# Kernel tuning notes

Hardware: AMD Instinct MI355X
Metric: run time of the kernel (lower is better)

## Reference

```python
import jax, jax.numpy as jnp
import numpy as np
from jax import lax

PI = jnp.pi
KX = jnp.array([[-1, 0, 1], [-2, 0, 2], [-1, 0, 1]], jnp.float32)
KY = jnp.array([[-1, -2, -1], [0, 0, 0], [1, 2, 1]], jnp.float32)
K45 = jnp.array([[-2, -1, 0], [-1, 0, 1], [0, 1, 2]], jnp.float32)
K135 = jnp.array([[0, 1, 2], [-1, 0, 1], [-2, -1, 0]], jnp.float32)


def _shift(x, dx, dy):
    # result[i, j] = x[clip(i - dx), clip(j - dy)]  (replicate boundary),
    # exactly matching the torch slice + replicate-pad neighbor construction.
    H, W = x.shape[2], x.shape[3]
    ri = jnp.clip(jnp.arange(H) - dx, 0, H - 1)
    ci = jnp.clip(jnp.arange(W) - dy, 0, W - 1)
    return x[:, :, ri[:, None], ci[None, :]]


def _adaptive_smoothing(f, k=10.0, iter_num=3):
    neighbors = [(-1, -1), (-1, 0), (-1, 1), (0, -1), (0, 0), (0, 1), (1, -1), (1, 0), (1, 1)]
    for _ in range(iter_num):
        Gx = (_shift(f, -1, 0) - _shift(f, 1, 0)) * 0.5   # gradient along H
        Gy = (_shift(f, 0, -1) - _shift(f, 0, 1)) * 0.5   # gradient along W
        w = jnp.exp(-(Gx * Gx + Gy * Gy) / (2.0 * k * k))
        f_new = jnp.zeros_like(f)
        w_sum = jnp.zeros_like(f)
        for dx, dy in neighbors:
            f_new = f_new + _shift(f, dx, dy) * _shift(w, dx, dy)
            w_sum = w_sum + _shift(w, dx, dy)
        f = f_new / jnp.maximum(w_sum, 1e-8)
    return f


def _dwconv(x, k2d):
    # depthwise 3x3 cross-correlation, zero padding (torch Conv2d semantics)
    C = x.shape[1]
    kern = jnp.broadcast_to(k2d[None, None], (C, 1, 3, 3)).astype(x.dtype)
    return lax.conv_general_dilated(x, kern, (1, 1), ((1, 1), (1, 1)),
                                    dimension_numbers=('NCHW', 'OIHW', 'NCHW'),
                                    feature_group_count=C)


def _sobel(x):
    return 0.5 * jnp.abs(_dwconv(x, KX)) + 0.5 * jnp.abs(_dwconv(x, KY))


def _hardswish(x):
    return x * jnp.clip(x + 3.0, 0.0, 6.0) / 6.0


def _canny(data, sigma, weight):
    blurred = _adaptive_smoothing(data, k=10.0, iter_num=3)
    sob = _sobel(blurred)
    B, C, H, W = sob.shape
    # torch.median: lower median = sorted[(n-1)//2]; .item() detaches it
    flat = jnp.sort(sob.reshape(B, C, H * W), axis=-1)
    med = lax.stop_gradient(jnp.mean(flat[:, :, (H * W - 1) // 2]))
    low = jnp.clip((1.0 - sigma) * med, 0.001, 1.0)
    high = jnp.clip((1.0 + sigma) * med, 0.001, 1.0)

    ex = _dwconv(blurred, KX)
    ey = _dwconv(blurred, KY)
    e45 = _dwconv(blurred, K45)
    e135 = _dwconv(blurred, K135)
    mag = jnp.sqrt(ex * ex + ey * ey + e45 * e45 + e135 * e135)
    ang = jnp.mod(jnp.arctan2(ey, ex), PI)

    dirs = jnp.array([0.0, PI / 4, PI / 2, 3 * PI / 4], jnp.float32)
    d = jnp.abs(ang[..., None] - dirs)
    dir_w = jax.nn.softmax(-jnp.minimum(d, PI - d) / 0.01, axis=-1)  # (B,C,H,W,4)

    pm = jnp.pad(mag, ((0, 0), (0, 0), (1, 1), (1, 1)), mode='edge')
    neigh = [(pm[:, :, 1:-1, :-2], pm[:, :, 1:-1, 2:]),
             (pm[:, :, :-2, :-2], pm[:, :, 2:, 2:]),
             (pm[:, :, :-2, 1:-1], pm[:, :, 2:, 1:-1]),
             (pm[:, :, :-2, 2:], pm[:, :, 2:, :-2])]
    sup = jnp.zeros_like(mag)
    for i, (n1, n2) in enumerate(neigh):  # fixed 4-direction loop
        sw = jax.nn.softmax(jnp.stack([mag, n1, n2], axis=-1) / 0.1, axis=-1)[..., 0]
        sup = sup + mag * sw * dir_w[..., i]

    mx = jnp.max(sup)
    sup = sup / jnp.where(mx > 0, mx, 1.0)

    Sh = _hardswish(sup - high)
    Sl = _hardswish(sup - low)
    ecanny = sup * (Sh + Sl)
    dilated = _dwconv(Sh, jnp.ones((3, 3), jnp.float32))
    result = ecanny + dilated * Sl * (1.0 - Sh)

    # enhance_edges with the ORIGINAL input
    result = (1.0 - weight) * result + weight * _sobel(data)
    rmin = jnp.min(result)
    rmax = jnp.max(result)
    return (result - rmin) / (rmax - rmin)


def setup_inputs() -> dict:
    key = jax.random.key(0)
    k1, k2 = jax.random.split(key)
    B, C, H, W = 8, 1, 512, 512
    return {
        'img1': jax.random.uniform(k1, (B, C, H, W), dtype=jnp.float32),
        'img2': jax.random.uniform(k2, (B, C, H, W), dtype=jnp.float32),
        'sigma1': jnp.float32(2.2),
        'enhance_weight1': jnp.float32(0.0),
        'sigma2': jnp.float32(2.2),
        'enhance_weight2': jnp.float32(0.0),
    }


def reference(img1, img2, sigma1, enhance_weight1, sigma2, enhance_weight2):
    s1 = 1.0 - jax.nn.sigmoid(sigma1)
    w1 = jax.nn.sigmoid(enhance_weight1)
    s2 = 1.0 - jax.nn.sigmoid(sigma2)
    w2 = jax.nn.sigmoid(enhance_weight2)
    m1 = _canny(img1, s1, w1)
    m2 = _canny(img2, s2, w2)
    f = (1.0 - m1) * (1.0 - m2) + m1 * m2
    return (1.0 - f, m1, m2)
```

## Files before the change

kernel.cpp:

```cpp
#include <hip/hip_runtime.h>

namespace {

constexpr int H = 512;
constexpr int W = 512;
constexpr int HW = H * W;
constexpr int PPS = 8;
constexpr int NP = 16;
constexpr int TX = 64;
constexpr int TY = 16;
constexpr int STY = 16;
constexpr int NBLK = (W / TX) * (H / TY) * NP;
constexpr float PI_F = 3.14159265358979323846f;
constexpr int NBINS = 1024;
constexpr float BIN_SCALE = 512.0f;

__device__ __forceinline__ float hsw(float x) {
    float t = fminf(fmaxf(x + 3.0f, 0.0f), 6.0f);
    return x * t * (1.0f / 6.0f);
}

__device__ __forceinline__ const float* plane_ptr(const float* s1, const float* s2, int p) {
    return (p < PPS) ? (s1 + (size_t)p * HW) : (s2 + (size_t)(p - PPS) * HW);
}

__device__ __forceinline__ float wave_max(float v) {
    for (int o = 32; o > 0; o >>= 1) v = fmaxf(v, __shfl_down(v, o, 64));
    return v;
}
__device__ __forceinline__ float wave_min(float v) {
    for (int o = 32; o > 0; o >>= 1) v = fminf(v, __shfl_down(v, o, 64));
    return v;
}

__device__ __forceinline__ float atan_poly(float t) {
    float z = t * t;
    float p = -0.01172120f;
    p = p * z + 0.05265332f;
    p = p * z - 0.11643287f;
    p = p * z + 0.19354346f;
    p = p * z - 0.33262347f;
    p = p * z + 0.99997726f;
    return t * p;
}

__device__ __forceinline__ float sel4(int idx, float v0, float v1, float v2, float v3) {
    float a = (idx & 1) ? v1 : v0;
    float b = (idx & 1) ? v3 : v2;
    return (idx & 2) ? b : a;
}

__global__ void K_smooth(const float* __restrict__ s1, const float* __restrict__ s2,
                         float* __restrict__ fout, unsigned* __restrict__ hist) {
    int tid = threadIdx.y * 64 + threadIdx.x;
    if (hist) {
        int bid = (blockIdx.z * gridDim.y + blockIdx.y) * gridDim.x + blockIdx.x;
        if (bid < (NP * NBINS) / 256) hist[bid * 256 + tid] = 0;
    }
    int p = blockIdx.z;
    const float* f = plane_ptr(s1, s2, p);
    int j0 = blockIdx.x * 64, i0 = blockIdx.y * STY;
    __shared__ float fs[STY + 4][68];
    __shared__ float ws[STY + 2][66];

    for (int e = tid; e < (STY + 4) * 68; e += 256) {
        int y = e / 68, x = e % 68;
        int gi = min(max(i0 - 2 + y, 0), H - 1);
        int gj = min(max(j0 - 2 + x, 0), W - 1);
        fs[y][x] = f[gi * W + gj];
    }
    __syncthreads();

    for (int e = tid; e < (STY + 2) * 66; e += 256) {
        int y = e / 66, x = e % 66;
        int r = min(max(i0 - 1 + y, 0), H - 1);
        int c = min(max(j0 - 1 + x, 0), W - 1);
        int yr = r - (i0 - 2), xc = c - (j0 - 2);
        int ym = max(r - 1, 0) - (i0 - 2), yp = min(r + 1, H - 1) - (i0 - 2);
        int xm = max(c - 1, 0) - (j0 - 2), xp = min(c + 1, W - 1) - (j0 - 2);
        float gx = 0.5f * (fs[yp][xc] - fs[ym][xc]);
        float gy = 0.5f * (fs[yr][xp] - fs[yr][xm]);
        ws[y][x] = __expf(-(gx * gx + gy * gy) * (1.0f / 200.0f));
    }
    __syncthreads();

    int yl = threadIdx.y * 4;
    int xl = threadIdx.x;
    float rn[6], rd[6];
#pragma unroll
    for (int k = 0; k < 6; k++) {
        float w0 = ws[yl + k][xl], w1 = ws[yl + k][xl + 1], w2 = ws[yl + k][xl + 2];
        float fA = fs[yl + k + 1][xl + 1], fB = fs[yl + k + 1][xl + 2], fC = fs[yl + k + 1][xl + 3];
        rn[k] = fA * w0 + fB * w1 + fC * w2;
        rd[k] = w0 + w1 + w2;
    }
    size_t base = (size_t)p * HW + (i0 + yl) * W + (j0 + xl);
#pragma unroll
    for (int k = 0; k < 4; k++) {
        fout[base + (size_t)k * W] =
            (rn[k] + rn[k + 1] + rn[k + 2]) / fmaxf(rd[k] + rd[k + 1] + rd[k + 2], 1e-8f);
    }
}

__global__ void K_dnms(const float* __restrict__ blur, float* __restrict__ sup,
                       unsigned* __restrict__ hist, float* __restrict__ pmax) {
    int p = blockIdx.z;
    const float* f = blur + (size_t)p * HW;
    int j0 = blockIdx.x * TX, i0 = blockIdx.y * TY;
    __shared__ float fs0[TY + 4][TX + 4];
    __shared__ float ms[TY + 2][TX + 2];
    __shared__ unsigned histS[NBINS];
    __shared__ float wred[4];
    int tid = threadIdx.y * 64 + threadIdx.x;

    for (int e = tid; e < NBINS; e += 256) histS[e] = 0;
    for (int e = tid; e < (TY + 4) * (TX + 4); e += 256) {
        int y = e / (TX + 4), x = e % (TX + 4);
        int gi = i0 - 2 + y, gj = j0 - 2 + x;
        fs0[y][x] = (gi >= 0 && gi < H && gj >= 0 && gj < W) ? f[gi * W + gj] : 0.0f;
    }
    __syncthreads();

    int xl = threadIdx.x;
    int yb = threadIdx.y * 4;

    float fv[6][3];
#pragma unroll
    for (int rr = 0; rr < 6; rr++)
#pragma unroll
        for (int cc = 0; cc < 3; cc++)
            fv[rr][cc] = fs0[yb + 1 + rr][xl + 1 + cc];

    float exk[4], eyk[4];
#pragma unroll
    for (int k = 0; k < 4; k++) {
        float xmm = fv[k][0], xm0 = fv[k][1], xmp = fv[k][2];
        float x0m = fv[k + 1][0], x0p = fv[k + 1][2];
        float xpm = fv[k + 2][0], xp0 = fv[k + 2][1], xpp = fv[k + 2][2];
        float ex = (xmp - xmm) + 2.0f * (x0p - x0m) + (xpp - xpm);
        float ey = (xpm + 2.0f * xp0 + xpp) - (xmm + 2.0f * xm0 + xmp);
        float e45 = -2.0f * xmm - xm0 - x0m + x0p + xp0 + 2.0f * xpp;
        float e135 = xm0 + 2.0f * xmp - x0m + x0p - 2.0f * xpm - xp0;
        ms[yb + 1 + k][xl + 1] = sqrtf(ex * ex + ey * ey + e45 * e45 + e135 * e135);
        exk[k] = ex;
        eyk[k] = ey;
    }

    if (tid < 2 * (TX + 2) + 2 * TY) {
        int y, x;
        if (tid < TX + 2) { y = 0; x = tid; }
        else if (tid < 2 * (TX + 2)) { y = TY + 1; x = tid - (TX + 2); }
        else if (tid < 2 * (TX + 2) + TY) { y = tid - 2 * (TX + 2) + 1; x = 0; }
        else { y = tid - (2 * (TX + 2) + TY) + 1; x = TX + 1; }
        int r = min(max(i0 - 1 + y, 0), H - 1);
        int c = min(max(j0 - 1 + x, 0), W - 1);
        int rr = r - i0 + 2, cc = c - j0 + 2;
        float xmm = fs0[rr - 1][cc - 1], xm0 = fs0[rr - 1][cc], xmp = fs0[rr - 1][cc + 1];
        float x0m = fs0[rr][cc - 1], x0p = fs0[rr][cc + 1];
        float xpm = fs0[rr + 1][cc - 1], xp0 = fs0[rr + 1][cc], xpp = fs0[rr + 1][cc + 1];
        float ex = (xmp - xmm) + 2.0f * (x0p - x0m) + (xpp - xpm);
        float ey = (xpm + 2.0f * xp0 + xpp) - (xmm + 2.0f * xm0 + xmp);
        float e45 = -2.0f * xmm - xm0 - x0m + x0p + xp0 + 2.0f * xpp;
        float e135 = xm0 + 2.0f * xmp - x0m + x0p - 2.0f * xpm - xp0;
        ms[y][x] = sqrtf(ex * ex + ey * ey + e45 * e45 + e135 * e135);
    }
    __syncthreads();

    float msr[6][3];
#pragma unroll
    for (int rr = 0; rr < 6; rr++)
#pragma unroll
        for (int cc = 0; cc < 3; cc++)
            msr[rr][cc] = ms[yb + rr][xl + cc];

    float bmax = 0.0f;
#pragma unroll
    for (int k = 0; k < 4; k++) {
        float ex = exk[k], ey = eyk[k];

        float ax = fabsf(ex), ay = fabsf(ey);
        float mn = fminf(ax, ay), mxv = fmaxf(ax, ay);
        float tq = (mxv > 0.0f) ? __fdividef(mn, mxv) : 0.0f;
        float pang = atan_poly(tq);
        if (ay > ax) pang = 1.57079632679f - pang;
        bool obtuse = ((__float_as_uint(ex) ^ __float_as_uint(ey)) & 0x80000000u) != 0u;
        float a = obtuse ? PI_F - pang : pang;

        float fa = a * 1.27323954474f;
        float nf = floorf(fa + 0.5f);
        float diff = a - nf * 0.78539816340f;
        float delta = fabsf(diff);
        int n = (int)nf & 3;
        int m = ((diff >= 0.0f) ? (int)nf + 1 : (int)nf - 1) & 3;
        float t = __expf(200.0f * delta - 78.5398163397f);
        float u = __fdividef(1.0f, 1.0f + t);

        float m0 = msr[k + 1][1];
        float n1a = msr[k + 1][0], n1b = msr[k][0], n1c = msr[k][1], n1d = msr[k][2];
        float n2a = msr[k + 1][2], n2b = msr[k + 2][2], n2c = msr[k + 2][1], n2d = msr[k + 2][0];
        float n1n = sel4(n, n1a, n1b, n1c, n1d);
        float n2n = sel4(n, n2a, n2b, n2c, n2d);
        float n1m = sel4(m, n1a, n1b, n1c, n1d);
        float n2m = sel4(m, n2a, n2b, n2c, n2d);

        float g1n = __expf((n1n - m0) * 10.0f);
        float g2n = __expf((n2n - m0) * 10.0f);
        float g1m = __expf((n1m - m0) * 10.0f);
        float g2m = __expf((n2m - m0) * 10.0f);
        float swn = __fdividef(1.0f, 1.0f + g1n + g2n);
        float swm = __fdividef(1.0f, 1.0f + g1m + g2m);
        float s = m0 * u * (swn + t * swm);

        sup[(size_t)p * HW + (i0 + yb + k) * W + (j0 + xl)] = s;
        bmax = fmaxf(bmax, s);

        float sv = 0.5f * (ax + ay);
        int bin = min((int)(sv * BIN_SCALE), NBINS - 1);
        atomicAdd(&histS[bin], 1u);
    }

    float wv = wave_max(bmax);
    if ((tid & 63) == 0) wred[tid >> 6] = wv;
    __syncthreads();
    if (tid == 0) {
        int bflat = (blockIdx.z * gridDim.y + blockIdx.y) * gridDim.x + blockIdx.x;
        pmax[bflat] = fmaxf(fmaxf(wred[0], wred[1]), fmaxf(wred[2], wred[3]));
    }
    for (int e = tid; e < NBINS; e += 256)
        if (histS[e]) atomicAdd(&hist[p * NBINS + e], histS[e]);
}

__global__ void K_stats(const unsigned* __restrict__ hist, const float* __restrict__ pmax,
                        float* __restrict__ medv, float* __restrict__ mx) {
    int b = blockIdx.x;
    int t = threadIdx.x;
    if (b < NP) {
        __shared__ unsigned sums[256];
        const unsigned* hp = hist + b * NBINS;
        unsigned s = 0;
        for (int q = 0; q < NBINS / 256; q++) s += hp[t * (NBINS / 256) + q];
        sums[t] = s;
        __syncthreads();
        for (int off = 1; off < 256; off <<= 1) {
            unsigned v = (t >= off) ? sums[t - off] : 0u;
            __syncthreads();
            sums[t] += v;
            __syncthreads();
        }
        const int k = (HW - 1) / 2;
        unsigned base = (t == 0) ? 0u : sums[t - 1];
        if ((int)base <= k && k < (int)sums[t]) {
            int cum = (int)base;
            int bin = t * (NBINS / 256);
            for (int q = 0; q < NBINS / 256; q++) {
                int c = (int)hp[t * (NBINS / 256) + q];
                if (cum + c > k) { bin = t * (NBINS / 256) + q; break; }
                cum += c;
            }
            medv[b] = ((float)bin + 0.5f) * (1.0f / BIN_SCALE);
        }
    } else {
        __shared__ float red[256];
        int s = b - NP;
        const float* base = pmax + s * (NBLK / 2);
        float v = -1e30f;
        for (int i = t; i < NBLK / 2; i += 256) v = fmaxf(v, base[i]);
        red[t] = v;
        __syncthreads();
        for (int sft = 128; sft > 0; sft >>= 1) {
            if (t < sft) red[t] = fmaxf(red[t], red[t + sft]);
            __syncthreads();
        }
        if (t == 0) mx[s] = red[0];
    }
}

__global__ void K_result(const float* __restrict__ sup, const float* __restrict__ im1,
                         const float* __restrict__ im2, const float* __restrict__ medv,
                         const float* __restrict__ sg1, const float* __restrict__ ew1,
                         const float* __restrict__ sg2, const float* __restrict__ ew2,
                         const float* __restrict__ mx, float* __restrict__ res,
                         float* __restrict__ prmax, float* __restrict__ prmin) {
    int p = blockIdx.z;
    int s = p >> 3;
    float med = 0.125f * (medv[s * PPS + 0] + medv[s * PPS + 1] + medv[s * PPS + 2] +
                          medv[s * PPS + 3] + medv[s * PPS + 4] + medv[s * PPS + 5] +
                          medv[s * PPS + 6] + medv[s * PPS + 7]);
    float sgin = (s == 0) ? sg1[0] : sg2[0];
    float ewin = (s == 0) ? ew1[0] : ew2[0];
    float sig = 1.0f - 1.0f / (1.0f + __expf(-sgin));
    float lo = fminf(fmaxf((1.0f - sig) * med, 0.001f), 1.0f);
    float hi = fminf(fmaxf((1.0f + sig) * med, 0.001f), 1.0f);
    float wg = 1.0f / (1.0f + __expf(-ewin));
    float m = mx[s];
    float inv = 1.0f / ((m > 0.0f) ? m : 1.0f);

    const float* sp = sup + (size_t)p * HW;
    const float* op = plane_ptr(im1, im2, p);
    int j0 = blockIdx.x * TX, i0 = blockIdx.y * TY;
    __shared__ float hs2[TY + 2][TX + 2];
    __shared__ float ssn[TY][TX];
    __shared__ float og[TY + 2][TX + 2];
    __shared__ float wredx[4], wredn[4];
    int tid = threadIdx.y * 64 + threadIdx.x;

    for (int e = tid; e < (TY + 2) * (TX + 2); e += 256) {
        int y = e / (TX + 2), x = e % (TX + 2);
        int gi = i0 - 1 + y, gj = j0 - 1 + x;
        float h = 0.0f, o = 0.0f;
        if (gi >= 0 && gi < H && gj >= 0 && gj < W) {
            float sv = sp[gi * W + gj] * inv;
            h = hsw(sv - hi);
            o = op[gi * W + gj];
            if (y >= 1 && y <= TY && x >= 1 && x <= TX) ssn[y - 1][x - 1] = sv;
        }
        hs2[y][x] = h;
        og[y][x] = o;
    }
    __syncthreads();

    int yl = threadIdx.y * 4;
    int xl = threadIdx.x;
    float hrow[6], ddr[6], ssr[6];
#pragma unroll
    for (int k = 0; k < 6; k++) {
        float a = hs2[yl + k][xl], bq = hs2[yl + k][xl + 1], c = hs2[yl + k][xl + 2];
        hrow[k] = a + bq + c;
        float oa = og[yl + k][xl], ob = og[yl + k][xl + 1], oc = og[yl + k][xl + 2];
        ddr[k] = oc - oa;
        ssr[k] = oa + 2.0f * ob + oc;
    }

    float bmx = -1e30f, bmn = 1e30f;
    size_t gbase = (size_t)p * HW + (i0 + yl) * W + (j0 + xl);
#pragma unroll
    for (int k = 0; k < 4; k++) {
        float sn = ssn[yl + k][xl];
        float Sh = hs2[yl + k + 1][xl + 1];
        float Sl = hsw(sn - lo);
        float dil = hrow[k] + hrow[k + 1] + hrow[k + 2];
        float pre = sn * (Sh + Sl) + dil * Sl * (1.0f - Sh);
        float sob = 0.5f * fabsf(ddr[k] + 2.0f * ddr[k + 1] + ddr[k + 2]) +
                    0.5f * fabsf(ssr[k + 2] - ssr[k]);
        float r = (1.0f - wg) * pre + wg * sob;
        res[gbase + (size_t)k * W] = r;
        bmx = fmaxf(bmx, r);
        bmn = fminf(bmn, r);
    }

    float vx = wave_max(bmx), vn = wave_min(bmn);
    if ((tid & 63) == 0) { wredx[tid >> 6] = vx; wredn[tid >> 6] = vn; }
    __syncthreads();
    if (tid == 0) {
        int bflat = (blockIdx.z * gridDim.y + blockIdx.y) * gridDim.x + blockIdx.x;
        prmax[bflat] = fmaxf(fmaxf(wredx[0], wredx[1]), fmaxf(wredx[2], wredx[3]));
        prmin[bflat] = fminf(fminf(wredn[0], wredn[1]), fminf(wredn[2], wredn[3]));
    }
}

__global__ void K_redminmax(const float* __restrict__ prmax, const float* __restrict__ prmin,
                            float* __restrict__ rmaxv, float* __restrict__ rminv) {
    __shared__ float rmx[256], rmn[256];
    int t = threadIdx.x;
    for (int s = 0; s < 2; s++) {
        const float* bx = prmax + s * (NBLK / 2);
        const float* bn = prmin + s * (NBLK / 2);
        float vx = -1e30f, vn = 1e30f;
        for (int i = t; i < NBLK / 2; i += 256) {
            vx = fmaxf(vx, bx[i]);
            vn = fminf(vn, bn[i]);
        }
        rmx[t] = vx;
        rmn[t] = vn;
        __syncthreads();
        for (int sft = 128; sft > 0; sft >>= 1) {
            if (t < sft) {
                rmx[t] = fmaxf(rmx[t], rmx[t + sft]);
                rmn[t] = fminf(rmn[t], rmn[t + sft]);
            }
            __syncthreads();
        }
        if (t == 0) { rmaxv[s] = rmx[0]; rminv[s] = rmn[0]; }
        __syncthreads();
    }
}

__global__ void K_final(const float* __restrict__ res, const float* __restrict__ rmaxv,
                        const float* __restrict__ rminv, float* __restrict__ out) {
    int j = blockIdx.x * 64 + threadIdx.x;
    int i = blockIdx.y * 4 + threadIdx.y;
    int p = blockIdx.z;
    float mx1 = rmaxv[0], mn1 = rminv[0];
    float mx2 = rmaxv[1], mn2 = rminv[1];
    size_t idx = (size_t)p * HW + i * W + j;
    float r1 = res[idx];
    float r2 = res[(size_t)(p + PPS) * HW + i * W + j];
    float m1 = (r1 - mn1) / (mx1 - mn1);
    float m2 = (r2 - mn2) / (mx2 - mn2);
    out[idx] = m1 + m2 - 2.0f * m1 * m2;
    out[(size_t)PPS * HW + idx] = m1;
    out[(size_t)2 * PPS * HW + idx] = m2;
}

}

extern "C" void kernel_launch(void* const* d_in, const int* in_sizes, int n_in,
                              void* d_out, int out_size, void* d_ws, size_t ws_size,
                              hipStream_t stream) {
    const float* img1 = (const float*)d_in[0];
    const float* img2 = (const float*)d_in[1];
    const float* sg1 = (const float*)d_in[2];
    const float* ew1 = (const float*)d_in[3];
    const float* sg2 = (const float*)d_in[4];
    const float* ew2 = (const float*)d_in[5];
    float* out = (float*)d_out;

    float* A = (float*)d_ws;
    float* B = A + (size_t)NP * HW;
    float* C = B + (size_t)NP * HW;
    unsigned* hist = (unsigned*)(C + (size_t)NP * HW);
    float* medv = (float*)(hist + NP * NBINS);
    float* mx = medv + NP;
    float* rmaxv = mx + 2;
    float* rminv = rmaxv + 2;
    float* pmax = rminv + 2;
    float* prmax = pmax + NBLK;
    float* prmin = prmax + NBLK;

    dim3 blk(64, 4, 1);
    dim3 grdT(W / TX, H / TY, NP);
    dim3 grdS(W / 64, H / STY, NP);
    dim3 grdF(W / 64, H / 4, PPS);
    dim3 mblk(256, 1, 1);

    K_smooth<<<grdS, blk, 0, stream>>>(img1, img2, A, hist);
    K_smooth<<<grdS, blk, 0, stream>>>(A, A + (size_t)PPS * HW, B, nullptr);
    K_smooth<<<grdS, blk, 0, stream>>>(B, B + (size_t)PPS * HW, A, nullptr);

    K_dnms<<<grdT, blk, 0, stream>>>(A, C, hist, pmax);

    K_stats<<<dim3(NP + 2), mblk, 0, stream>>>(hist, pmax, medv, mx);

    K_result<<<grdT, blk, 0, stream>>>(C, img1, img2, medv, sg1, ew1, sg2, ew2, mx,
                                       B, prmax, prmin);
    K_redminmax<<<dim3(1), mblk, 0, stream>>>(prmax, prmin, rmaxv, rminv);
    K_final<<<grdF, blk, 0, stream>>>(B, rmaxv, rminv, out);
}
```

Baseline: 120.0 us.

## Fold min/max reduction into final kernel, vectorize it, add interior fast paths

Removes the single-block K_redminmax launch. Each K_final block now redundantly reduces the per-block min/max partials itself, then writes normalized outputs with float4 loads and stores, four rows per thread. The smoothing, NMS and result kernels gain an interior-tile path that skips the clamped or bounds-checked index math during halo loads. The trade is that every K_final block repeats the partial reduction over NBLK/2 entries per image set, and the code carries duplicated branches.

```diff
diff --git a/kernel.cpp b/kernel.cpp
--- a/kernel.cpp
+++ b/kernel.cpp
@@ -11,6 +11,7 @@
 constexpr int TY = 16;
 constexpr int STY = 16;
 constexpr int NBLK = (W / TX) * (H / TY) * NP;
+constexpr int HBLK = NBLK / 2;
 constexpr float PI_F = 3.14159265358979323846f;
 constexpr int NBINS = 1024;
 constexpr float BIN_SCALE = 512.0f;
@@ -63,24 +64,40 @@
     __shared__ float fs[STY + 4][68];
     __shared__ float ws[STY + 2][66];
 
-    for (int e = tid; e < (STY + 4) * 68; e += 256) {
-        int y = e / 68, x = e % 68;
-        int gi = min(max(i0 - 2 + y, 0), H - 1);
-        int gj = min(max(j0 - 2 + x, 0), W - 1);
-        fs[y][x] = f[gi * W + gj];
-    }
-    __syncthreads();
-
-    for (int e = tid; e < (STY + 2) * 66; e += 256) {
-        int y = e / 66, x = e % 66;
-        int r = min(max(i0 - 1 + y, 0), H - 1);
-        int c = min(max(j0 - 1 + x, 0), W - 1);
-        int yr = r - (i0 - 2), xc = c - (j0 - 2);
-        int ym = max(r - 1, 0) - (i0 - 2), yp = min(r + 1, H - 1) - (i0 - 2);
-        int xm = max(c - 1, 0) - (j0 - 2), xp = min(c + 1, W - 1) - (j0 - 2);
-        float gx = 0.5f * (fs[yp][xc] - fs[ym][xc]);
-        float gy = 0.5f * (fs[yr][xp] - fs[yr][xm]);
-        ws[y][x] = __expf(-(gx * gx + gy * gy) * (1.0f / 200.0f));
+    bool interior = (i0 >= 2) && (i0 + STY + 1 <= H - 1) && (j0 >= 2) && (j0 + 65 <= W - 1);
+
+    if (interior) {
+        const float* fb = f + (i0 - 2) * W + (j0 - 2);
+        for (int e = tid; e < (STY + 4) * 68; e += 256) {
+            int y = e / 68, x = e % 68;
+            fs[y][x] = fb[y * W + x];
+        }
+        __syncthreads();
+        for (int e = tid; e < (STY + 2) * 66; e += 256) {
+            int y = e / 66, x = e % 66;
+            float gx = 0.5f * (fs[y + 2][x + 1] - fs[y][x + 1]);
+            float gy = 0.5f * (fs[y + 1][x + 2] - fs[y + 1][x]);
+            ws[y][x] = __expf(-(gx * gx + gy * gy) * (1.0f / 200.0f));
+        }
+    } else {
+        for (int e = tid; e < (STY + 4) * 68; e += 256) {
+            int y = e / 68, x = e % 68;
+            int gi = min(max(i0 - 2 + y, 0), H - 1);
+            int gj = min(max(j0 - 2 + x, 0), W - 1);
+            fs[y][x] = f[gi * W + gj];
+        }
+        __syncthreads();
+        for (int e = tid; e < (STY + 2) * 66; e += 256) {
+            int y = e / 66, x = e % 66;
+            int r = min(max(i0 - 1 + y, 0), H - 1);
+            int c = min(max(j0 - 1 + x, 0), W - 1);
+            int yr = r - (i0 - 2), xc = c - (j0 - 2);
+            int ym = max(r - 1, 0) - (i0 - 2), yp = min(r + 1, H - 1) - (i0 - 2);
+            int xm = max(c - 1, 0) - (j0 - 2), xp = min(c + 1, W - 1) - (j0 - 2);
+            float gx = 0.5f * (fs[yp][xc] - fs[ym][xc]);
+            float gy = 0.5f * (fs[yr][xp] - fs[yr][xm]);
+            ws[y][x] = __expf(-(gx * gx + gy * gy) * (1.0f / 200.0f));
+        }
     }
     __syncthreads();
 
@@ -113,11 +130,21 @@
     __shared__ float wred[4];
     int tid = threadIdx.y * 64 + threadIdx.x;
 
+    bool interior = (i0 >= 2) && (i0 + TY + 1 <= H - 1) && (j0 >= 2) && (j0 + TX + 1 <= W - 1);
+
     for (int e = tid; e < NBINS; e += 256) histS[e] = 0;
-    for (int e = tid; e < (TY + 4) * (TX + 4); e += 256) {
-        int y = e / (TX + 4), x = e % (TX + 4);
-        int gi = i0 - 2 + y, gj = j0 - 2 + x;
-        fs0[y][x] = (gi >= 0 && gi < H && gj >= 0 && gj < W) ? f[gi * W + gj] : 0.0f;
+    if (interior) {
+        const float* fb = f + (i0 - 2) * W + (j0 - 2);
+        for (int e = tid; e < (TY + 4) * (TX + 4); e += 256) {
+            int y = e / (TX + 4), x = e % (TX + 4);
+            fs0[y][x] = fb[y * W + x];
+        }
+    } else {
+        for (int e = tid; e < (TY + 4) * (TX + 4); e += 256) {
+            int y = e / (TX + 4), x = e % (TX + 4);
+            int gi = i0 - 2 + y, gj = j0 - 2 + x;
+            fs0[y][x] = (gi >= 0 && gi < H && gj >= 0 && gj < W) ? f[gi * W + gj] : 0.0f;
+        }
     }
     __syncthreads();
 
@@ -152,9 +179,13 @@
         else if (tid < 2 * (TX + 2)) { y = TY + 1; x = tid - (TX + 2); }
         else if (tid < 2 * (TX + 2) + TY) { y = tid - 2 * (TX + 2) + 1; x = 0; }
         else { y = tid - (2 * (TX + 2) + TY) + 1; x = TX + 1; }
-        int r = min(max(i0 - 1 + y, 0), H - 1);
-        int c = min(max(j0 - 1 + x, 0), W - 1);
-        int rr = r - i0 + 2, cc = c - j0 + 2;
+        int rr, cc;
+        if (interior) { rr = y + 1; cc = x + 1; }
+        else {
+            int r = min(max(i0 - 1 + y, 0), H - 1);
+            int c = min(max(j0 - 1 + x, 0), W - 1);
+            rr = r - i0 + 2; cc = c - j0 + 2;
+        }
         float xmm = fs0[rr - 1][cc - 1], xm0 = fs0[rr - 1][cc], xmp = fs0[rr - 1][cc + 1];
         float x0m = fs0[rr][cc - 1], x0p = fs0[rr][cc + 1];
         float xpm = fs0[rr + 1][cc - 1], xp0 = fs0[rr + 1][cc], xpp = fs0[rr + 1][cc + 1];
@@ -262,9 +293,9 @@
     } else {
         __shared__ float red[256];
         int s = b - NP;
-        const float* base = pmax + s * (NBLK / 2);
+        const float* base = pmax + s * HBLK;
         float v = -1e30f;
-        for (int i = t; i < NBLK / 2; i += 256) v = fmaxf(v, base[i]);
+        for (int i = t; i < HBLK; i += 256) v = fmaxf(v, base[i]);
         red[t] = v;
         __syncthreads();
         for (int sft = 128; sft > 0; sft >>= 1) {
@@ -304,18 +335,32 @@
     __shared__ float wredx[4], wredn[4];
     int tid = threadIdx.y * 64 + threadIdx.x;
 
-    for (int e = tid; e < (TY + 2) * (TX + 2); e += 256) {
-        int y = e / (TX + 2), x = e % (TX + 2);
-        int gi = i0 - 1 + y, gj = j0 - 1 + x;
-        float h = 0.0f, o = 0.0f;
-        if (gi >= 0 && gi < H && gj >= 0 && gj < W) {
-            float sv = sp[gi * W + gj] * inv;
-            h = hsw(sv - hi);
-            o = op[gi * W + gj];
+    bool interior = (i0 >= 1) && (i0 + TY <= H - 1) && (j0 >= 1) && (j0 + TX <= W - 1);
+
+    if (interior) {
+        const float* spb = sp + (i0 - 1) * W + (j0 - 1);
+        const float* opb = op + (i0 - 1) * W + (j0 - 1);
+        for (int e = tid; e < (TY + 2) * (TX + 2); e += 256) {
+            int y = e / (TX + 2), x = e % (TX + 2);
+            float sv = spb[y * W + x] * inv;
+            hs2[y][x] = hsw(sv - hi);
+            og[y][x] = opb[y * W + x];
             if (y >= 1 && y <= TY && x >= 1 && x <= TX) ssn[y - 1][x - 1] = sv;
         }
-        hs2[y][x] = h;
-        og[y][x] = o;
+    } else {
+        for (int e = tid; e < (TY + 2) * (TX + 2); e += 256) {
+            int y = e / (TX + 2), x = e % (TX + 2);
+            int gi = i0 - 1 + y, gj = j0 - 1 + x;
+            float h = 0.0f, o = 0.0f;
+            if (gi >= 0 && gi < H && gj >= 0 && gj < W) {
+                float sv = sp[gi * W + gj] * inv;
+                h = hsw(sv - hi);
+                o = op[gi * W + gj];
+                if (y >= 1 && y <= TY && x >= 1 && x <= TX) ssn[y - 1][x - 1] = sv;
+            }
+            hs2[y][x] = h;
+            og[y][x] = o;
+        }
     }
     __syncthreads();
 
@@ -358,48 +403,59 @@
     }
 }
 
-__global__ void K_redminmax(const float* __restrict__ prmax, const float* __restrict__ prmin,
-                            float* __restrict__ rmaxv, float* __restrict__ rminv) {
-    __shared__ float rmx[256], rmn[256];
-    int t = threadIdx.x;
-    for (int s = 0; s < 2; s++) {
-        const float* bx = prmax + s * (NBLK / 2);
-        const float* bn = prmin + s * (NBLK / 2);
-        float vx = -1e30f, vn = 1e30f;
-        for (int i = t; i < NBLK / 2; i += 256) {
-            vx = fmaxf(vx, bx[i]);
-            vn = fminf(vn, bn[i]);
-        }
-        rmx[t] = vx;
-        rmn[t] = vn;
-        __syncthreads();
-        for (int sft = 128; sft > 0; sft >>= 1) {
-            if (t < sft) {
-                rmx[t] = fmaxf(rmx[t], rmx[t + sft]);
-                rmn[t] = fminf(rmn[t], rmn[t + sft]);
-            }
-            __syncthreads();
-        }
-        if (t == 0) { rmaxv[s] = rmx[0]; rminv[s] = rmn[0]; }
-        __syncthreads();
-    }
-}
-
-__global__ void K_final(const float* __restrict__ res, const float* __restrict__ rmaxv,
-                        const float* __restrict__ rminv, float* __restrict__ out) {
-    int j = blockIdx.x * 64 + threadIdx.x;
-    int i = blockIdx.y * 4 + threadIdx.y;
+__global__ void K_final(const float* __restrict__ res, const float* __restrict__ prmax,
+                        const float* __restrict__ prmin, float* __restrict__ out) {
+    int tid = threadIdx.y * 64 + threadIdx.x;
+
+    float vx0 = -1e30f, vn0 = 1e30f, vx1 = -1e30f, vn1 = 1e30f;
+    for (int i = tid; i < HBLK; i += 256) {
+        vx0 = fmaxf(vx0, prmax[i]);
+        vn0 = fminf(vn0, prmin[i]);
+        vx1 = fmaxf(vx1, prmax[HBLK + i]);
+        vn1 = fminf(vn1, prmin[HBLK + i]);
+    }
+    vx0 = wave_max(vx0); vn0 = wave_min(vn0);
+    vx1 = wave_max(vx1); vn1 = wave_min(vn1);
+    __shared__ float sx0[4], sn0[4], sx1[4], sn1[4];
+    if ((tid & 63) == 0) {
+        int w = tid >> 6;
+        sx0[w] = vx0; sn0[w] = vn0; sx1[w] = vx1; sn1[w] = vn1;
+    }
+    __syncthreads();
+    float mx1 = fmaxf(fmaxf(sx0[0], sx0[1]), fmaxf(sx0[2], sx0[3]));
+    float mn1 = fminf(fminf(sn0[0], sn0[1]), fminf(sn0[2], sn0[3]));
+    float mx2 = fmaxf(fmaxf(sx1[0], sx1[1]), fmaxf(sx1[2], sx1[3]));
+    float mn2 = fminf(fminf(sn1[0], sn1[1]), fminf(sn1[2], sn1[3]));
+    float is1 = 1.0f / (mx1 - mn1);
+    float is2 = 1.0f / (mx2 - mn2);
+
+    int col4 = blockIdx.x * 64 + threadIdx.x;
+    int i0 = blockIdx.y * 16 + threadIdx.y * 4;
     int p = blockIdx.z;
-    float mx1 = rmaxv[0], mn1 = rminv[0];
-    float mx2 = rmaxv[1], mn2 = rminv[1];
-    size_t idx = (size_t)p * HW + i * W + j;
-    float r1 = res[idx];
-    float r2 = res[(size_t)(p + PPS) * HW + i * W + j];
-    float m1 = (r1 - mn1) / (mx1 - mn1);
-    float m2 = (r2 - mn2) / (mx2 - mn2);
-    out[idx] = m1 + m2 - 2.0f * m1 * m2;
-    out[(size_t)PPS * HW + idx] = m1;
-    out[(size_t)2 * PPS * HW + idx] = m2;
+    const float4* r1p = (const float4*)(res + (size_t)p * HW);
+    const float4* r2p = (const float4*)(res + (size_t)(p + PPS) * HW);
+    float4* outc = (float4*)(out) + (size_t)p * (HW / 4);
+    float4* out1 = (float4*)(out) + (size_t)(PPS + p) * (HW / 4);
+    float4* out2 = (float4*)(out) + (size_t)(2 * PPS + p) * (HW / 4);
+
+#pragma unroll
+    for (int k = 0; k < 4; k++) {
+        int row = i0 + k;
+        float4 a = r1p[row * (W / 4) + col4];
+        float4 b = r2p[row * (W / 4) + col4];
+        float4 m1v, m2v, mcv;
+        m1v.x = (a.x - mn1) * is1; m1v.y = (a.y - mn1) * is1;
+        m1v.z = (a.z - mn1) * is1; m1v.w = (a.w - mn1) * is1;
+        m2v.x = (b.x - mn2) * is2; m2v.y = (b.y - mn2) * is2;
+        m2v.z = (b.z - mn2) * is2; m2v.w = (b.w - mn2) * is2;
+        mcv.x = m1v.x + m2v.x - 2.0f * m1v.x * m2v.x;
+        mcv.y = m1v.y + m2v.y - 2.0f * m1v.y * m2v.y;
+        mcv.z = m1v.z + m2v.z - 2.0f * m1v.z * m2v.z;
+        mcv.w = m1v.w + m2v.w - 2.0f * m1v.w * m2v.w;
+        outc[row * (W / 4) + col4] = mcv;
+        out1[row * (W / 4) + col4] = m1v;
+        out2[row * (W / 4) + col4] = m2v;
+    }
 }
 
 }
@@ -421,16 +477,14 @@
     unsigned* hist = (unsigned*)(C + (size_t)NP * HW);
     float* medv = (float*)(hist + NP * NBINS);
     float* mx = medv + NP;
-    float* rmaxv = mx + 2;
-    float* rminv = rmaxv + 2;
-    float* pmax = rminv + 2;
+    float* pmax = mx + 2;
     float* prmax = pmax + NBLK;
     float* prmin = prmax + NBLK;
 
     dim3 blk(64, 4, 1);
     dim3 grdT(W / TX, H / TY, NP);
     dim3 grdS(W / 64, H / STY, NP);
-    dim3 grdF(W / 64, H / 4, PPS);
+    dim3 grdF(W / 256, H / 16, PPS);
     dim3 mblk(256, 1, 1);
 
     K_smooth<<<grdS, blk, 0, stream>>>(img1, img2, A, hist);
@@ -443,6 +497,6 @@
 
     K_result<<<grdT, blk, 0, stream>>>(C, img1, img2, medv, sg1, ew1, sg2, ew2, mx,
                                        B, prmax, prmin);
-    K_redminmax<<<dim3(1), mblk, 0, stream>>>(prmax, prmin, rmaxv, rminv);
-    K_final<<<grdF, blk, 0, stream>>>(B, rmaxv, rminv, out);
-}
+
+    K_final<<<grdF, blk, 0, stream>>>(B, prmax, prmin, out);
+}
```

New measurement: 112.3 us. 1.07x faster.
